# Kernel tuning notes

Hardware: AMD Instinct MI355X
Metric: run time of the kernel (lower is better)

## Reference

```python
import jax, jax.numpy as jnp
import numpy as np

N_NODES = 100000
N_EDGES = 1000000
F_DIM = 128


def setup_inputs() -> dict:
    key = jax.random.key(0)
    ks = jax.random.split(key, 12)
    s = lambda k, shape: jax.random.normal(k, shape, dtype=jnp.float32) * (1.0 / np.sqrt(shape[0]))
    return {
        "x": jax.random.normal(ks[0], (N_NODES, F_DIM), dtype=jnp.float32),
        "edge_index": jax.random.randint(ks[1], (2, N_EDGES), 0, N_NODES, dtype=jnp.int64),
        "W1": s(ks[2], (2 * F_DIM, 64)), "b1": jnp.zeros((64,), jnp.float32), "A1": s(ks[3], (2 * F_DIM, 64)),
        "W2": s(ks[4], (64, 32)), "b2": jnp.zeros((32,), jnp.float32), "A2": s(ks[5], (64, 32)),
        "W3": s(ks[6], (32, 16)), "b3": jnp.zeros((16,), jnp.float32), "A3": s(ks[7], (32, 16)),
        "Wf": s(ks[8], (16, 1)), "bf": jnp.zeros((1,), jnp.float32),
    }


def _res_block(h, W, b, A):
    # out = relu(h @ W + b); residual = h @ A (bias-free adjust); return relu(out + residual)
    out = jax.nn.relu(h @ W + b)
    return jax.nn.relu(out + h @ A)


def reference(x, edge_index, W1, b1, A1, W2, b2, A2, W3, b3, A3, Wf, bf):
    # NOTE: in the original forward, the GNN output is overwritten by data.x,
    # so the effective computation is gather -> concat -> residual MLP -> sigmoid.
    src, dst = edge_index[0], edge_index[1]
    h = jnp.concatenate([x[src], x[dst]], axis=-1)  # [E, 2F]
    h = _res_block(h, W1, b1, A1)  # [E, 64]
    h = _res_block(h, W2, b2, A2)  # [E, 32]
    h = _res_block(h, W3, b3, A3)  # [E, 16]
    return jax.nn.sigmoid(h @ Wf + bf)  # [E, 1]
```

## Files before the change

kernel.cpp:

```cpp
#include <hip/hip_runtime.h>
#include <stdint.h>

#define E_TOTAL 1000000
#define N_NODES 100000
#define FD      128
#define ETILE   64
#define NTILES  (E_TOTAL / ETILE)
#define GRID    3125
#define KTILES  5

typedef __attribute__((ext_vector_type(8))) short short8;
typedef __attribute__((ext_vector_type(4))) short short4v;
typedef __attribute__((ext_vector_type(4))) float f32x4;

__device__ __forceinline__ short f2bf(float f) {
  union { float f; unsigned u; } v; v.f = f;
  unsigned r = (v.u + 0x7FFFu + ((v.u >> 16) & 1u)) >> 16;
  return (short)(r & 0xFFFFu);
}

__global__ __launch_bounds__(256)
void convert_x_kernel(const float* __restrict__ x, short* __restrict__ xb) {
  const int i = (blockIdx.x * 256 + threadIdx.x) * 8;
  float4 a = *(const float4*)(x + i);
  float4 b = *(const float4*)(x + i + 4);
  short8 s;
  s[0] = f2bf(a.x); s[1] = f2bf(a.y); s[2] = f2bf(a.z); s[3] = f2bf(a.w);
  s[4] = f2bf(b.x); s[5] = f2bf(b.y); s[6] = f2bf(b.z); s[7] = f2bf(b.w);
  *(short8*)(xb + i) = s;
}

template <bool USEBF>
__global__ __launch_bounds__(256, 2)
void linkpred_kernel(const float* __restrict__ x,
                     const short* __restrict__ xbf,
                     const int* __restrict__ ei,
                     const float* __restrict__ W1, const float* __restrict__ b1,
                     const float* __restrict__ A1,
                     const float* __restrict__ W2, const float* __restrict__ b2,
                     const float* __restrict__ A2,
                     const float* __restrict__ W3, const float* __restrict__ b3,
                     const float* __restrict__ A3,
                     const float* __restrict__ Wf, const float* __restrict__ bfp,
                     float* __restrict__ out)
{
  __shared__ __align__(16) char R[ETILE * 264 * 2];
  __shared__ int SIDX[2][ETILE];

  short (*H0)[264] = (short(*)[264])R;
  short (*H1)[72]  = (short(*)[72])R;
  short (*H2)[40]  = (short(*)[40])(R + 16384);

  const int tid  = threadIdx.x;
  const int w    = tid >> 6;
  const int lane = tid & 63;
  const int col  = lane & 15;
  const int quad = lane >> 4;

  short8 B1f[2][8];
  for (int p = 0; p < 2; ++p) {
    const int n = 16 * (w + 4 * p) + col;
    const float* src = (p == 0) ? (W1 + n) : (A1 + (n - 64));
    for (int kt = 0; kt < 8; ++kt) {
      short8 f;
      for (int j = 0; j < 8; ++j)
        f[j] = f2bf(src[(kt * 32 + quad * 8 + j) * 64]);
      B1f[p][kt] = f;
    }
  }
  short8 B2f[2][2];
  for (int p = 0; p < 2; ++p) {
    const int n = 16 * ((w & 1) + 2 * p) + col;
    const float* src = (p == 0) ? (W2 + n) : (A2 + (n - 32));
    for (int kt = 0; kt < 2; ++kt) {
      short8 f;
      for (int j = 0; j < 8; ++j)
        f[j] = f2bf(src[(kt * 32 + quad * 8 + j) * 32]);
      B2f[p][kt] = f;
    }
  }
  short8 B3f[2];
  for (int p = 0; p < 2; ++p) {
    const int n = 16 * p + col;
    const float* src = (p == 0) ? (W3 + n) : (A3 + (n - 16));
    short8 f;
    for (int j = 0; j < 8; ++j)
      f[j] = f2bf(src[(quad * 8 + j) * 16]);
    B3f[p] = f;
  }
  const float b1v = b1[16 * w + col];
  const float b2v = b2[16 * (w & 1) + col];
  const float b3v = b3[col];
  const float bfv = bfp[0];
  const float wfv = Wf[col];
  const f32x4 zero = {0.f, 0.f, 0.f, 0.f};

  {
    const int e0 = blockIdx.x * ETILE;
    if (tid < 2 * ETILE)
      SIDX[tid >> 6][tid & 63] = ei[(tid >> 6) * E_TOTAL + e0 + (tid & 63)];
  }
  __syncthreads();

  int tile = blockIdx.x;
  for (int k = 0; k < KTILES; ++k, tile += GRID) {
    const int e0 = tile * ETILE;

    int nxt = 0;
    const bool pf = (tid < 2 * ETILE) && (k < KTILES - 1);
    if (pf) nxt = ei[(tid >> 6) * E_TOTAL + (e0 + GRID * ETILE) + (tid & 63)];

    if (USEBF) {
      short4v g[16];
#pragma unroll
      for (int it = 0; it < 16; ++it) {
        const int e    = it * 4 + w;
        const int node = SIDX[lane >> 5][e];
        g[it] = *(const short4v*)(xbf + (size_t)node * FD + (lane & 31) * 4);
      }
#pragma unroll
      for (int it = 0; it < 16; ++it) {
        const int e = it * 4 + w;
        *(short4v*)&H0[e][(lane >> 5) * FD + (lane & 31) * 4] = g[it];
      }
    } else {
      for (int it = 0; it < ETILE / 4; ++it) {
        const int e    = it * 4 + w;
        const int node = SIDX[lane >> 5][e];
        const int cc   = lane & 31;
        float4 v = ((const float4*)(x + (size_t)node * FD))[cc];
        short4v s;
        s[0] = f2bf(v.x); s[1] = f2bf(v.y); s[2] = f2bf(v.z); s[3] = f2bf(v.w);
        *(short4v*)&H0[e][lane * 4] = s;
      }
    }
    __syncthreads();

    if (pf) SIDX[tid >> 6][tid & 63] = nxt;

    f32x4 acc[4][2];
    for (int mt = 0; mt < 4; ++mt) { acc[mt][0] = zero; acc[mt][1] = zero; }
    for (int kt = 0; kt < 8; ++kt) {
      for (int mt = 0; mt < 4; ++mt) {
        short8 a = *(const short8*)&H0[mt * 16 + col][kt * 32 + quad * 8];
        acc[mt][0] = __builtin_amdgcn_mfma_f32_16x16x32_bf16(a, B1f[0][kt], acc[mt][0], 0, 0, 0);
        acc[mt][1] = __builtin_amdgcn_mfma_f32_16x16x32_bf16(a, B1f[1][kt], acc[mt][1], 0, 0, 0);
      }
    }
    __syncthreads();

    for (int mt = 0; mt < 4; ++mt)
      for (int r = 0; r < 4; ++r) {
        float o = fmaxf(acc[mt][0][r] + b1v, 0.f);
        float h = fmaxf(o + acc[mt][1][r], 0.f);
        H1[mt * 16 + quad * 4 + r][16 * w + col] = f2bf(h);
      }
    __syncthreads();

    f32x4 acc2[2][2];
    acc2[0][0] = zero; acc2[0][1] = zero; acc2[1][0] = zero; acc2[1][1] = zero;
    for (int kt = 0; kt < 2; ++kt)
      for (int mi = 0; mi < 2; ++mi) {
        const int m = (2 * (w >> 1) + mi) * 16 + col;
        short8 a = *(const short8*)&H1[m][kt * 32 + quad * 8];
        acc2[mi][0] = __builtin_amdgcn_mfma_f32_16x16x32_bf16(a, B2f[0][kt], acc2[mi][0], 0, 0, 0);
        acc2[mi][1] = __builtin_amdgcn_mfma_f32_16x16x32_bf16(a, B2f[1][kt], acc2[mi][1], 0, 0, 0);
      }
    for (int mi = 0; mi < 2; ++mi)
      for (int r = 0; r < 4; ++r) {
        float o = fmaxf(acc2[mi][0][r] + b2v, 0.f);
        float h = fmaxf(o + acc2[mi][1][r], 0.f);
        H2[(2 * (w >> 1) + mi) * 16 + quad * 4 + r][16 * (w & 1) + col] = f2bf(h);
      }
    __syncthreads();

    f32x4 acc3[2];
    acc3[0] = zero; acc3[1] = zero;
    {
      short8 a = *(const short8*)&H2[w * 16 + col][quad * 8];
      acc3[0] = __builtin_amdgcn_mfma_f32_16x16x32_bf16(a, B3f[0], acc3[0], 0, 0, 0);
      acc3[1] = __builtin_amdgcn_mfma_f32_16x16x32_bf16(a, B3f[1], acc3[1], 0, 0, 0);
    }

    float4 res;
    float* resp = (float*)&res;
    for (int r = 0; r < 4; ++r) {
      float o = fmaxf(acc3[0][r] + b3v, 0.f);
      float h = fmaxf(o + acc3[1][r], 0.f);
      float s = h * wfv;
      s += __shfl_xor(s, 1, 16);
      s += __shfl_xor(s, 2, 16);
      s += __shfl_xor(s, 4, 16);
      s += __shfl_xor(s, 8, 16);
      resp[r] = 1.0f / (1.0f + __expf(-(s + bfv)));
    }
    if (col == 0)
      *(float4*)(out + e0 + w * 16 + quad * 4) = res;

    __syncthreads();
  }
}

extern "C" void kernel_launch(void* const* d_in, const int* in_sizes, int n_in,
                              void* d_out, int out_size, void* d_ws, size_t ws_size,
                              hipStream_t stream) {
  const float* x   = (const float*)d_in[0];
  const int*   ei  = (const int*)d_in[1];
  const float* W1  = (const float*)d_in[2];
  const float* b1  = (const float*)d_in[3];
  const float* A1  = (const float*)d_in[4];
  const float* W2  = (const float*)d_in[5];
  const float* b2  = (const float*)d_in[6];
  const float* A2  = (const float*)d_in[7];
  const float* W3  = (const float*)d_in[8];
  const float* b3  = (const float*)d_in[9];
  const float* A3  = (const float*)d_in[10];
  const float* Wf  = (const float*)d_in[11];
  const float* bfp = (const float*)d_in[12];

  const size_t xb_bytes = (size_t)N_NODES * FD * sizeof(short);

  if (ws_size >= xb_bytes) {
    short* xb = (short*)d_ws;
    hipLaunchKernelGGL(convert_x_kernel, dim3(N_NODES * FD / (256 * 8)), dim3(256), 0, stream,
                       x, xb);
    hipLaunchKernelGGL((linkpred_kernel<true>), dim3(GRID), dim3(256), 0, stream,
                       x, (const short*)xb, ei, W1, b1, A1, W2, b2, A2, W3, b3, A3, Wf, bfp,
                       (float*)d_out);
  } else {
    hipLaunchKernelGGL((linkpred_kernel<false>), dim3(GRID), dim3(256), 0, stream,
                       x, (const short*)nullptr, ei, W1, b1, A1, W2, b2, A2, W3, b3, A3, Wf, bfp,
                       (float*)d_out);
  }
}
```

Baseline: 246.7 us.

## Software-pipeline node-feature gathers across tiles using register-held indices

Edge indices are now loaded into registers per wave and broadcast with shuffles instead of staged through shared memory. The gather of the next tile's node features is issued right after the current tile is written to LDS, so the global loads overlap with the three MFMA layers. The index load for the tile after that is prefetched two tiles ahead. This raises register pressure, since 16 gathered vectors stay live across the GEMMs, which could hurt occupancy under launch_bounds(256,2).

Result: no change. 248.6 us (+0.7%).

```diff
diff --git a/kernel.cpp b/kernel.cpp
--- a/kernel.cpp
+++ b/kernel.cpp
@@ -45,7 +45,6 @@
                      float* __restrict__ out)
 {
   __shared__ __align__(16) char R[ETILE * 264 * 2];
-  __shared__ int SIDX[2][ETILE];
 
   short (*H0)[264] = (short(*)[264])R;
   short (*H1)[72]  = (short(*)[72])R;
@@ -95,29 +94,36 @@
   const float wfv = Wf[col];
   const f32x4 zero = {0.f, 0.f, 0.f, 0.f};
 
-  {
-    const int e0 = blockIdx.x * ETILE;
-    if (tid < 2 * ETILE)
-      SIDX[tid >> 6][tid & 63] = ei[(tid >> 6) * E_TOTAL + e0 + (tid & 63)];
-  }
-  __syncthreads();
+  auto load_idx = [&](int tile) -> int {
+    int v = 0;
+    if (lane < 32) {
+      const int half = lane & 1, j = lane >> 1;
+      v = ei[half * E_TOTAL + tile * ETILE + j * 4 + w];
+    }
+    return v;
+  };
+
+  short4v g[16];
+  auto issue_gather = [&](int idxreg) {
+#pragma unroll
+    for (int it = 0; it < 16; ++it) {
+      const int node = __shfl(idxreg, it * 2 + (lane >> 5));
+      g[it] = *(const short4v*)(xbf + (size_t)node * FD + (lane & 31) * 4);
+    }
+  };
+
+  int idx_nxt = 0;
+  if (USEBF) {
+    int idx0 = load_idx(blockIdx.x);
+    issue_gather(idx0);
+    idx_nxt = load_idx(blockIdx.x + GRID);
+  }
 
   int tile = blockIdx.x;
   for (int k = 0; k < KTILES; ++k, tile += GRID) {
     const int e0 = tile * ETILE;
 
-    int nxt = 0;
-    const bool pf = (tid < 2 * ETILE) && (k < KTILES - 1);
-    if (pf) nxt = ei[(tid >> 6) * E_TOTAL + (e0 + GRID * ETILE) + (tid & 63)];
-
     if (USEBF) {
-      short4v g[16];
-#pragma unroll
-      for (int it = 0; it < 16; ++it) {
-        const int e    = it * 4 + w;
-        const int node = SIDX[lane >> 5][e];
-        g[it] = *(const short4v*)(xbf + (size_t)node * FD + (lane & 31) * 4);
-      }
 #pragma unroll
       for (int it = 0; it < 16; ++it) {
         const int e = it * 4 + w;
@@ -126,7 +132,7 @@
     } else {
       for (int it = 0; it < ETILE / 4; ++it) {
         const int e    = it * 4 + w;
-        const int node = SIDX[lane >> 5][e];
+        const int node = ei[(lane >> 5) * E_TOTAL + e0 + e];
         const int cc   = lane & 31;
         float4 v = ((const float4*)(x + (size_t)node * FD))[cc];
         short4v s;
@@ -136,7 +142,10 @@
     }
     __syncthreads();
 
-    if (pf) SIDX[tid >> 6][tid & 63] = nxt;
+    if (USEBF && (k + 1 < KTILES)) {
+      issue_gather(idx_nxt);
+      if (k + 2 < KTILES) idx_nxt = load_idx(tile + 2 * GRID);
+    }
 
     f32x4 acc[4][2];
     for (int mt = 0; mt < 4; ++mt) { acc[mt][0] = zero; acc[mt][1] = zero; }
```
